# Kernel optimization log

Measured on AMD Instinct MI355X. Metric: run time of the kernel, lower is better.

## Reference

```python
import jax, jax.numpy as jnp
import numpy as np

N_NODES = 50000
N_EDGES = 800000
IN_F, OUT_F, N_HEADS = 128, 64, 4
NEG_SLOPE = 0.2
EPS = 1e-12


def setup_inputs() -> dict:
    key = jax.random.key(0)
    ks = jax.random.split(key, 6)
    x = jax.random.normal(ks[0], (N_NODES, IN_F), dtype=jnp.float32)
    edge_index = jax.random.randint(ks[1], (2, N_EDGES), 0, N_NODES, dtype=jnp.int32)
    # xavier-uniform-like scaled params
    W = jax.random.normal(ks[2], (IN_F, OUT_F), dtype=jnp.float32) * (2.0 / (IN_F + OUT_F)) ** 0.5
    a_l = jax.random.normal(ks[3], (OUT_F, N_HEADS), dtype=jnp.float32) * (2.0 / (OUT_F + N_HEADS)) ** 0.5
    a_r = jax.random.normal(ks[4], (OUT_F, N_HEADS), dtype=jnp.float32) * (2.0 / (OUT_F + N_HEADS)) ** 0.5
    b = jnp.zeros((OUT_F,), dtype=jnp.float32)
    return {"x": x, "edge_index": edge_index, "W": W, "a_l": a_l, "a_r": a_r, "b": b}


def reference(x, edge_index, W, a_l, a_r, b):
    # GATConv forward (eval mode: attn dropout is identity).
    # Dense NxNxH scatter + L1 normalize in the original == per-row edge softmax
    # over exp(leaky_relu(el[row]+er[col])); honor edge sparsity directly.
    n = x.shape[0]
    h = x @ W                      # [N, D] node representations
    el = h @ a_l                   # [N, H] left (dst/row) scores
    er = h @ a_r                   # [N, H] right (src/col) scores
    row, col = edge_index[0], edge_index[1]
    e = el[row] + er[col]          # [E, H]
    e = jnp.where(e > 0, e, NEG_SLOPE * e)   # leaky_relu(0.2)
    e = jnp.exp(e)
    denom = jax.ops.segment_sum(e, row, num_segments=n)        # [N, H]
    attn = e / jnp.maximum(denom[row], EPS)                    # [E, H] L1-normalized per row
    msg = attn[:, :, None] * h[col][:, None, :]                # [E, H, D]
    out = jax.ops.segment_sum(msg, row, num_segments=n)        # [N, H, D]
    out = out + b                                              # bias broadcast over heads
    return out.reshape(n, -1)                                  # [N, H*D]
```

## Files before the change

### kernel.cpp

```cpp
#include <hip/hip_runtime.h>

#define N_NODES 50000
#define N_EDGES 800000
#define IN_F    128
#define OUT_F   64
#define N_HEADS 4
#define NEG_SLOPE 0.2f
#define EPS 1e-12f

#define NODE_BLOCKS 782
#define NB   196
#define NCH  784
#define S2N  (NB * NCH)
#define S2B  151

typedef __attribute__((ext_vector_type(8))) short bf16x8;
typedef __attribute__((ext_vector_type(4))) float f32x4;

__device__ __forceinline__ unsigned short f2bf(float f) {
    unsigned int u = __float_as_uint(f);
    u += 0x7FFFu + ((u >> 16) & 1u);
    return (unsigned short)(u >> 16);
}

__global__ __launch_bounds__(256) void k_init(
    const float* __restrict__ W, unsigned short* __restrict__ Wt,
    const int* __restrict__ row, int* __restrict__ histG)
{
    __shared__ int hist[NB];
    const int bb = blockIdx.x;
    const int t = threadIdx.x;
    if (bb < 4) {
        int i = bb * 256 + t;
        for (; i < OUT_F * IN_F; i += 4 * 256) {
            int c = i >> 7, k = i & 127;
            Wt[i] = f2bf(W[k * OUT_F + c]);
        }
        return;
    }
    const int ch = bb - 4;
    if (t < NB) hist[t] = 0;
    __syncthreads();
    const int e0 = ch * 1024 + t * 4;
    if (e0 + 3 < N_EDGES) {
        int4 r4 = *(const int4*)(row + e0);
        atomicAdd(&hist[r4.x >> 8], 1);
        atomicAdd(&hist[r4.y >> 8], 1);
        atomicAdd(&hist[r4.z >> 8], 1);
        atomicAdd(&hist[r4.w >> 8], 1);
    } else {
        #pragma unroll
        for (int j = 0; j < 4; ++j)
            if (e0 + j < N_EDGES) atomicAdd(&hist[row[e0 + j] >> 8], 1);
    }
    __syncthreads();
    if (t < NB) histG[t * NCH + ch] = hist[t];
}

__global__ __launch_bounds__(256) void k_h_el_er(
    const float* __restrict__ x, const unsigned short* __restrict__ Wt,
    const float* __restrict__ a_l, const float* __restrict__ a_r,
    unsigned short* __restrict__ h_bf,
    float* __restrict__ el, float* __restrict__ er)
{
    __shared__ unsigned short xs[64 * 128];
    __shared__ unsigned short wsh[64 * 128];
    const int tid = threadIdx.x;
    const int node0 = blockIdx.x * 64;

    {
        const uint4* src = (const uint4*)Wt;
        #pragma unroll
        for (int j = 0; j < 4; ++j) {
            int idx = tid + 256 * j;
            int r = idx >> 4;
            int cb = (idx & 15) << 4;
            uint4 v = src[idx];
            *(uint4*)((char*)wsh + r * 256 + (cb ^ ((r & 7) << 4))) = v;
        }
    }
    {
        const int r = tid >> 2;
        const int c0 = (tid & 3) * 32;
        const int node = node0 + r;
        unsigned int pk[16];
        if (node < N_NODES) {
            const float* src = x + (size_t)node * IN_F + c0;
            #pragma unroll
            for (int i = 0; i < 8; ++i) {
                float4 v = *(const float4*)(src + 4 * i);
                pk[2 * i + 0] = (unsigned)f2bf(v.x) | ((unsigned)f2bf(v.y) << 16);
                pk[2 * i + 1] = (unsigned)f2bf(v.z) | ((unsigned)f2bf(v.w) << 16);
            }
        } else {
            #pragma unroll
            for (int i = 0; i < 16; ++i) pk[i] = 0;
        }
        #pragma unroll
        for (int q = 0; q < 4; ++q) {
            int cb = c0 * 2 + q * 16;
            *(uint4*)((char*)xs + r * 256 + (cb ^ ((r & 7) << 4))) =
                make_uint4(pk[4 * q], pk[4 * q + 1], pk[4 * q + 2], pk[4 * q + 3]);
        }
    }
    __syncthreads();

    const int w  = tid >> 6, l = tid & 63;
    const int lr = l & 15, lg = l >> 4;
    const int arow = w * 16 + lr;

    bf16x8 afr[4];
    #pragma unroll
    for (int t = 0; t < 4; ++t) {
        int cb = t * 64 + lg * 16;
        afr[t] = *(const bf16x8*)((char*)xs + arow * 256 + (cb ^ ((arow & 7) << 4)));
    }

    const f32x4 zero = {0.f, 0.f, 0.f, 0.f};
    f32x4 acc[4] = {zero, zero, zero, zero};
    #pragma unroll
    for (int nt = 0; nt < 4; ++nt) {
        const int brow = nt * 16 + lr;
        #pragma unroll
        for (int t = 0; t < 4; ++t) {
            int cb = t * 64 + lg * 16;
            bf16x8 bfr = *(const bf16x8*)((char*)wsh + brow * 256 + (cb ^ ((brow & 7) << 4)));
            acc[nt] = __builtin_amdgcn_mfma_f32_16x16x32_bf16(afr[t], bfr, acc[nt], 0, 0, 0);
        }
    }

    #pragma unroll
    for (int r = 0; r < 4; ++r) {
        const int node = node0 + w * 16 + lg * 4 + r;
        if (node < N_NODES) {
            #pragma unroll
            for (int nt = 0; nt < 4; ++nt)
                h_bf[(size_t)node * OUT_F + nt * 16 + lr] = f2bf(acc[nt][r]);
        }
    }

    float4 al4[4], ar4[4];
    #pragma unroll
    for (int nt = 0; nt < 4; ++nt) {
        al4[nt] = *(const float4*)(a_l + (size_t)(nt * 16 + lr) * N_HEADS);
        ar4[nt] = *(const float4*)(a_r + (size_t)(nt * 16 + lr) * N_HEADS);
    }
    #pragma unroll
    for (int r = 0; r < 4; ++r) {
        float4 pl = make_float4(0.f, 0.f, 0.f, 0.f);
        float4 pr = make_float4(0.f, 0.f, 0.f, 0.f);
        #pragma unroll
        for (int nt = 0; nt < 4; ++nt) {
            const float v = acc[nt][r];
            pl.x += v * al4[nt].x; pl.y += v * al4[nt].y;
            pl.z += v * al4[nt].z; pl.w += v * al4[nt].w;
            pr.x += v * ar4[nt].x; pr.y += v * ar4[nt].y;
            pr.z += v * ar4[nt].z; pr.w += v * ar4[nt].w;
        }
        #pragma unroll
        for (int off = 1; off < 16; off <<= 1) {
            pl.x += __shfl_xor(pl.x, off); pl.y += __shfl_xor(pl.y, off);
            pl.z += __shfl_xor(pl.z, off); pl.w += __shfl_xor(pl.w, off);
            pr.x += __shfl_xor(pr.x, off); pr.y += __shfl_xor(pr.y, off);
            pr.z += __shfl_xor(pr.z, off); pr.w += __shfl_xor(pr.w, off);
        }
        const int node = node0 + w * 16 + lg * 4 + r;
        if (lr == 0 && node < N_NODES) {
            *(float4*)(el + (size_t)node * N_HEADS) = pl;
            *(float4*)(er + (size_t)node * N_HEADS) = pr;
        }
    }
}

__global__ __launch_bounds__(256) void k_scan2_local(
    const int* __restrict__ histG, int* __restrict__ scanHist,
    int* __restrict__ blocksum)
{
    __shared__ int wsum[4];
    const int t = threadIdx.x;
    const int base = blockIdx.x * 1024 + t * 4;

    int4 d = make_int4(0, 0, 0, 0);
    if (base + 3 < S2N) d = *(const int4*)(histG + base);
    else {
        if (base + 0 < S2N) d.x = histG[base + 0];
        if (base + 1 < S2N) d.y = histG[base + 1];
        if (base + 2 < S2N) d.z = histG[base + 2];
        if (base + 3 < S2N) d.w = histG[base + 3];
    }
    const int tsum = d.x + d.y + d.z + d.w;

    const int lane = t & 63, wave = t >> 6;
    int inc = tsum;
    #pragma unroll
    for (int off = 1; off < 64; off <<= 1) {
        int v = __shfl_up(inc, off);
        if (lane >= off) inc += v;
    }
    if (lane == 63) wsum[wave] = inc;
    __syncthreads();

    int woff = 0;
    #pragma unroll
    for (int w = 0; w < 4; ++w) woff += (w < wave) ? wsum[w] : 0;

    const int ex = woff + inc - tsum;
    int4 o;
    o.x = ex; o.y = ex + d.x; o.z = o.y + d.y; o.w = o.z + d.z;
    if (base + 3 < S2N) *(int4*)(scanHist + base) = o;
    else {
        if (base + 0 < S2N) scanHist[base + 0] = o.x;
        if (base + 1 < S2N) scanHist[base + 1] = o.y;
        if (base + 2 < S2N) scanHist[base + 2] = o.z;
        if (base + 3 < S2N) scanHist[base + 3] = o.w;
    }
    if (t == 0) blocksum[blockIdx.x] = wsum[0] + wsum[1] + wsum[2] + wsum[3];
}

__global__ __launch_bounds__(256) void k_scan2_add(
    const int* __restrict__ blocksum, int* __restrict__ scanHist)
{
    const int bb = blockIdx.x;
    int off = 0;
    for (int i = 0; i < bb; ++i) off += blocksum[i];
    if (off == 0) return;

    const int t = threadIdx.x;
    const int base = bb * 1024 + t * 4;
    if (base + 3 < S2N) {
        int4 v = *(int4*)(scanHist + base);
        v.x += off; v.y += off; v.z += off; v.w += off;
        *(int4*)(scanHist + base) = v;
    } else {
        if (base + 0 < S2N) scanHist[base + 0] += off;
        if (base + 1 < S2N) scanHist[base + 1] += off;
        if (base + 2 < S2N) scanHist[base + 2] += off;
        if (base + 3 < S2N) scanHist[base + 3] += off;
    }
}

__global__ __launch_bounds__(256) void k_scatter(
    const int* __restrict__ row, const int* __restrict__ col,
    const int* __restrict__ scanHist, unsigned* __restrict__ ebuf)
{
    __shared__ int off[NB];
    const int ch = blockIdx.x;
    const int t = threadIdx.x;
    if (t < NB) off[t] = scanHist[t * NCH + ch];
    __syncthreads();
    const int e0 = ch * 1024;
    #pragma unroll
    for (int k = 0; k < 4; ++k) {
        const int e = e0 + t + k * 256;
        if (e < N_EDGES) {
            const int r = row[e], c = col[e];
            const int pos = atomicAdd(&off[r >> 8], 1);
            ebuf[pos] = ((unsigned)(r & 255) << 17) | (unsigned)c;
        }
    }
}

__global__ __launch_bounds__(256) void k_bucket(
    const unsigned* __restrict__ ebuf, const int* __restrict__ scanHist,
    int* __restrict__ rowptr, int* __restrict__ csr_col)
{
    __shared__ int cnt[256];
    __shared__ int wsum[4];
    const int b = blockIdx.x;
    const int t = threadIdx.x;
    const int base = scanHist[b * NCH];
    const int end  = (b < NB - 1) ? scanHist[(b + 1) * NCH] : N_EDGES;

    cnt[t] = 0;
    __syncthreads();
    for (int i = base + t; i < end; i += 256)
        atomicAdd(&cnt[ebuf[i] >> 17], 1);
    __syncthreads();

    const int val = cnt[t];
    const int lane = t & 63, wave = t >> 6;
    int inc = val;
    #pragma unroll
    for (int off = 1; off < 64; off <<= 1) {
        int v = __shfl_up(inc, off);
        if (lane >= off) inc += v;
    }
    if (lane == 63) wsum[wave] = inc;
    __syncthreads();
    int woff = 0;
    #pragma unroll
    for (int w = 0; w < 4; ++w) woff += (w < wave) ? wsum[w] : 0;
    const int excl = base + woff + inc - val;

    const int node = (b << 8) + t;
    if (node < N_NODES) rowptr[node] = excl;
    if (b == NB - 1 && t == 0) rowptr[N_NODES] = N_EDGES;
    __syncthreads();
    cnt[t] = excl;
    __syncthreads();

    for (int i = base + t; i < end; i += 256) {
        const unsigned p = ebuf[i];
        const int pos = atomicAdd(&cnt[p >> 17], 1);
        csr_col[pos] = (int)(p & 0x1FFFFu);
    }
}

__global__ __launch_bounds__(256) void k_gather(
    const int* __restrict__ rowptr, const int* __restrict__ csr_col,
    const float* __restrict__ el, const float* __restrict__ er,
    const unsigned short* __restrict__ h_bf, const float* __restrict__ b,
    float* __restrict__ out)
{
    int n = blockIdx.x * 4 + (threadIdx.x >> 6);
    if (n >= N_NODES) return;
    const int lane = threadIdx.x & 63;
    const int g    = lane >> 4;
    const int fq   = lane & 15;

    const int s0 = rowptr[n], s1 = rowptr[n + 1];
    const int deg = s1 - s0;
    const int nit = (deg + 3) >> 2;

    float acc[4][4];
    #pragma unroll
    for (int hd = 0; hd < 4; ++hd)
        #pragma unroll
        for (int f = 0; f < 4; ++f) acc[hd][f] = 0.f;
    float den[4] = {0.f, 0.f, 0.f, 0.f};

    const float4 elv = *reinterpret_cast<const float4*>(el + ((unsigned)n << 2));

    bool v_cur = false;
    float4 erv_cur = make_float4(0.f, 0.f, 0.f, 0.f);
    uint2  h_cur = make_uint2(0, 0);
    if (nit > 0) {
        const int j = s0 + g;
        v_cur = j < s1;
        const int jc = v_cur ? j : (s1 - 1);
        const int c = csr_col[jc];
        erv_cur = *reinterpret_cast<const float4*>(er + ((unsigned)c << 2));
        h_cur   = *reinterpret_cast<const uint2*>(h_bf + (((unsigned)c << 6) + (fq << 2)));
    }

    for (int it = 0; it < nit; ++it) {
        bool v_nx = false;
        float4 erv_nx = make_float4(0.f, 0.f, 0.f, 0.f);
        uint2  h_nx = make_uint2(0, 0);
        if (it + 1 < nit) {
            const int j = s0 + (it + 1) * 4 + g;
            v_nx = j < s1;
            const int jc = v_nx ? j : (s1 - 1);
            const int c = csr_col[jc];
            erv_nx = *reinterpret_cast<const float4*>(er + ((unsigned)c << 2));
            h_nx   = *reinterpret_cast<const uint2*>(h_bf + (((unsigned)c << 6) + (fq << 2)));
        }

        float t0 = elv.x + erv_cur.x, t1 = elv.y + erv_cur.y;
        float t2 = elv.z + erv_cur.z, t3 = elv.w + erv_cur.w;
        t0 = t0 > 0.f ? t0 : NEG_SLOPE * t0;
        t1 = t1 > 0.f ? t1 : NEG_SLOPE * t1;
        t2 = t2 > 0.f ? t2 : NEG_SLOPE * t2;
        t3 = t3 > 0.f ? t3 : NEG_SLOPE * t3;
        float4 w = make_float4(__expf(t0), __expf(t1), __expf(t2), __expf(t3));
        if (!v_cur) w = make_float4(0.f, 0.f, 0.f, 0.f);

        const float h0 = __uint_as_float(h_cur.x << 16);
        const float h1 = __uint_as_float(h_cur.x & 0xFFFF0000u);
        const float h2 = __uint_as_float(h_cur.y << 16);
        const float h3 = __uint_as_float(h_cur.y & 0xFFFF0000u);

        den[0] += w.x; den[1] += w.y; den[2] += w.z; den[3] += w.w;
        acc[0][0] += w.x * h0; acc[0][1] += w.x * h1; acc[0][2] += w.x * h2; acc[0][3] += w.x * h3;
        acc[1][0] += w.y * h0; acc[1][1] += w.y * h1; acc[1][2] += w.y * h2; acc[1][3] += w.y * h3;
        acc[2][0] += w.z * h0; acc[2][1] += w.z * h1; acc[2][2] += w.z * h2; acc[2][3] += w.z * h3;
        acc[3][0] += w.w * h0; acc[3][1] += w.w * h1; acc[3][2] += w.w * h2; acc[3][3] += w.w * h3;

        v_cur = v_nx; erv_cur = erv_nx; h_cur = h_nx;
    }

    #pragma unroll
    for (int hd = 0; hd < 4; ++hd) {
        float v = den[hd];
        v += __shfl_xor(v, 16); v += __shfl_xor(v, 32);
        den[hd] = v;
        #pragma unroll
        for (int f = 0; f < 4; ++f) {
            float u = acc[hd][f];
            u += __shfl_xor(u, 16); u += __shfl_xor(u, 32);
            acc[hd][f] = u;
        }
    }

    const float dg = g == 0 ? den[0] : g == 1 ? den[1] : g == 2 ? den[2] : den[3];
    const float inv = 1.f / fmaxf(dg, EPS);
    float4 o;
    o.x = (g == 0 ? acc[0][0] : g == 1 ? acc[1][0] : g == 2 ? acc[2][0] : acc[3][0]);
    o.y = (g == 0 ? acc[0][1] : g == 1 ? acc[1][1] : g == 2 ? acc[2][1] : acc[3][1]);
    o.z = (g == 0 ? acc[0][2] : g == 1 ? acc[1][2] : g == 2 ? acc[2][2] : acc[3][2]);
    o.w = (g == 0 ? acc[0][3] : g == 1 ? acc[1][3] : g == 2 ? acc[2][3] : acc[3][3]);

    const float4 bias = *(const float4*)(b + fq * 4);
    o.x = o.x * inv + bias.x;
    o.y = o.y * inv + bias.y;
    o.z = o.z * inv + bias.z;
    o.w = o.w * inv + bias.w;
    *(float4*)(out + (size_t)n * (N_HEADS * OUT_F) + g * 64 + fq * 4) = o;
}

extern "C" void kernel_launch(void* const* d_in, const int* in_sizes, int n_in,
                              void* d_out, int out_size, void* d_ws, size_t ws_size,
                              hipStream_t stream)
{
    const float* x   = (const float*)d_in[0];
    const int*   ei  = (const int*)d_in[1];
    const float* W   = (const float*)d_in[2];
    const float* a_l = (const float*)d_in[3];
    const float* a_r = (const float*)d_in[4];
    const float* b   = (const float*)d_in[5];
    float* out = (float*)d_out;

    char* ws = (char*)d_ws;
    unsigned short* h_bf = (unsigned short*)(ws);
    float*    el       = (float*)   (ws +  6400000);
    float*    er       = (float*)   (ws +  7200000);
    unsigned short* Wt = (unsigned short*)(ws + 8000000);
    int*      histG    = (int*)     (ws +  8016384);
    int*      scanHist = (int*)     (ws +  8631040);
    int*      blocksum = (int*)     (ws +  9245696);
    unsigned* ebuf     = (unsigned*)(ws +  9246720);
    int*      csr_col  = (int*)     (ws + 12446720);
    int*      rowptr   = (int*)     (ws + 15646720);

    const int* row = ei;
    const int* col = ei + N_EDGES;

    k_init      <<<4 + NCH, 256, 0, stream>>>(W, Wt, row, histG);
    k_h_el_er   <<<NODE_BLOCKS, 256, 0, stream>>>(x, Wt, a_l, a_r, h_bf, el, er);
    k_scan2_local<<<S2B, 256, 0, stream>>>(histG, scanHist, blocksum);
    k_scan2_add <<<S2B, 256, 0, stream>>>(blocksum, scanHist);
    k_scatter   <<<NCH, 256, 0, stream>>>(row, col, scanHist, ebuf);
    k_bucket    <<<NB, 256, 0, stream>>>(ebuf, scanHist, rowptr, csr_col);
    k_gather    <<<N_NODES / 4, 256, 0, stream>>>(rowptr, csr_col, el, er, h_bf, b, out);
}
```

Measured before the change: 93.54 us.

## Precompute edge attention weights in bucket pass and deepen gather prefetch

```diff
diff --git a/kernel.cpp b/kernel.cpp
--- a/kernel.cpp
+++ b/kernel.cpp
@@ -9,10 +9,11 @@
 #define EPS 1e-12f
 
 #define NODE_BLOCKS 782
-#define NB   196
-#define NCH  784
-#define S2N  (NB * NCH)
-#define S2B  151
+#define NB    391
+#define CHUNK 2048
+#define NCH   391
+#define S2N   (NB * NCH)
+#define S2B   150
 
 typedef __attribute__((ext_vector_type(8))) short bf16x8;
 typedef __attribute__((ext_vector_type(4))) float f32x4;
@@ -39,22 +40,23 @@
         return;
     }
     const int ch = bb - 4;
-    if (t < NB) hist[t] = 0;
-    __syncthreads();
-    const int e0 = ch * 1024 + t * 4;
-    if (e0 + 3 < N_EDGES) {
-        int4 r4 = *(const int4*)(row + e0);
-        atomicAdd(&hist[r4.x >> 8], 1);
-        atomicAdd(&hist[r4.y >> 8], 1);
-        atomicAdd(&hist[r4.z >> 8], 1);
-        atomicAdd(&hist[r4.w >> 8], 1);
+    for (int i = t; i < NB; i += 256) hist[i] = 0;
+    __syncthreads();
+    const int e0 = ch * CHUNK + t * 8;
+    if (e0 + 7 < N_EDGES) {
+        int4 a = *(const int4*)(row + e0);
+        int4 c = *(const int4*)(row + e0 + 4);
+        atomicAdd(&hist[a.x >> 7], 1); atomicAdd(&hist[a.y >> 7], 1);
+        atomicAdd(&hist[a.z >> 7], 1); atomicAdd(&hist[a.w >> 7], 1);
+        atomicAdd(&hist[c.x >> 7], 1); atomicAdd(&hist[c.y >> 7], 1);
+        atomicAdd(&hist[c.z >> 7], 1); atomicAdd(&hist[c.w >> 7], 1);
     } else {
         #pragma unroll
-        for (int j = 0; j < 4; ++j)
-            if (e0 + j < N_EDGES) atomicAdd(&hist[row[e0 + j] >> 8], 1);
-    }
-    __syncthreads();
-    if (t < NB) histG[t * NCH + ch] = hist[t];
+        for (int j = 0; j < 8; ++j)
+            if (e0 + j < N_EDGES) atomicAdd(&hist[row[e0 + j] >> 7], 1);
+    }
+    __syncthreads();
+    for (int i = t; i < NB; i += 256) histG[i * NCH + ch] = hist[i];
 }
 
 __global__ __launch_bounds__(256) void k_h_el_er(
@@ -246,69 +248,92 @@
     __shared__ int off[NB];
     const int ch = blockIdx.x;
     const int t = threadIdx.x;
-    if (t < NB) off[t] = scanHist[t * NCH + ch];
-    __syncthreads();
-    const int e0 = ch * 1024;
-    #pragma unroll
-    for (int k = 0; k < 4; ++k) {
+    for (int i = t; i < NB; i += 256) off[i] = scanHist[i * NCH + ch];
+    __syncthreads();
+    const int e0 = ch * CHUNK;
+    #pragma unroll
+    for (int k = 0; k < 8; ++k) {
         const int e = e0 + t + k * 256;
         if (e < N_EDGES) {
             const int r = row[e], c = col[e];
-            const int pos = atomicAdd(&off[r >> 8], 1);
-            ebuf[pos] = ((unsigned)(r & 255) << 17) | (unsigned)c;
+            const int pos = atomicAdd(&off[r >> 7], 1);
+            ebuf[pos] = ((unsigned)(r & 127) << 17) | (unsigned)c;
         }
     }
 }
 
 __global__ __launch_bounds__(256) void k_bucket(
     const unsigned* __restrict__ ebuf, const int* __restrict__ scanHist,
-    int* __restrict__ rowptr, int* __restrict__ csr_col)
-{
-    __shared__ int cnt[256];
-    __shared__ int wsum[4];
+    const float* __restrict__ el, const float* __restrict__ er,
+    int* __restrict__ rowptr, int* __restrict__ csr_col,
+    float4* __restrict__ csr_w)
+{
+    __shared__ float4 elv[128];
+    __shared__ int cnt[128];
+    __shared__ int wsum2[2];
     const int b = blockIdx.x;
     const int t = threadIdx.x;
+    const int node0 = b << 7;
     const int base = scanHist[b * NCH];
     const int end  = (b < NB - 1) ? scanHist[(b + 1) * NCH] : N_EDGES;
 
-    cnt[t] = 0;
+    if (t < 128) {
+        const int node = node0 + t;
+        elv[t] = (node < N_NODES) ? *(const float4*)(el + node * 4)
+                                  : make_float4(0.f, 0.f, 0.f, 0.f);
+        cnt[t] = 0;
+    }
     __syncthreads();
     for (int i = base + t; i < end; i += 256)
         atomicAdd(&cnt[ebuf[i] >> 17], 1);
     __syncthreads();
 
-    const int val = cnt[t];
+    int inc = 0, val = 0;
     const int lane = t & 63, wave = t >> 6;
-    int inc = val;
-    #pragma unroll
-    for (int off = 1; off < 64; off <<= 1) {
-        int v = __shfl_up(inc, off);
-        if (lane >= off) inc += v;
-    }
-    if (lane == 63) wsum[wave] = inc;
-    __syncthreads();
-    int woff = 0;
-    #pragma unroll
-    for (int w = 0; w < 4; ++w) woff += (w < wave) ? wsum[w] : 0;
-    const int excl = base + woff + inc - val;
-
-    const int node = (b << 8) + t;
-    if (node < N_NODES) rowptr[node] = excl;
+    if (t < 128) {
+        val = cnt[t];
+        inc = val;
+        #pragma unroll
+        for (int off = 1; off < 64; off <<= 1) {
+            int v = __shfl_up(inc, off);
+            if (lane >= off) inc += v;
+        }
+        if (lane == 63) wsum2[wave] = inc;
+    }
+    __syncthreads();
+    int excl = 0;
+    if (t < 128) {
+        const int woff = (wave == 1) ? wsum2[0] : 0;
+        excl = base + woff + inc - val;
+        const int node = node0 + t;
+        if (node < N_NODES) rowptr[node] = excl;
+    }
     if (b == NB - 1 && t == 0) rowptr[N_NODES] = N_EDGES;
     __syncthreads();
-    cnt[t] = excl;
+    if (t < 128) cnt[t] = excl;
     __syncthreads();
 
     for (int i = base + t; i < end; i += 256) {
         const unsigned p = ebuf[i];
-        const int pos = atomicAdd(&cnt[p >> 17], 1);
-        csr_col[pos] = (int)(p & 0x1FFFFu);
+        const int r = p >> 17;
+        const int c = (int)(p & 0x1FFFFu);
+        const int pos = atomicAdd(&cnt[r], 1);
+        const float4 e4 = elv[r];
+        const float4 r4 = *(const float4*)(er + ((unsigned)c << 2));
+        float s0 = e4.x + r4.x, s1 = e4.y + r4.y;
+        float s2 = e4.z + r4.z, s3 = e4.w + r4.w;
+        s0 = s0 > 0.f ? s0 : NEG_SLOPE * s0;
+        s1 = s1 > 0.f ? s1 : NEG_SLOPE * s1;
+        s2 = s2 > 0.f ? s2 : NEG_SLOPE * s2;
+        s3 = s3 > 0.f ? s3 : NEG_SLOPE * s3;
+        csr_col[pos] = c;
+        csr_w[pos] = make_float4(__expf(s0), __expf(s1), __expf(s2), __expf(s3));
     }
 }
 
 __global__ __launch_bounds__(256) void k_gather(
     const int* __restrict__ rowptr, const int* __restrict__ csr_col,
-    const float* __restrict__ el, const float* __restrict__ er,
+    const float4* __restrict__ csr_w,
     const unsigned short* __restrict__ h_bf, const float* __restrict__ b,
     float* __restrict__ out)
 {
@@ -319,8 +344,7 @@
     const int fq   = lane & 15;
 
     const int s0 = rowptr[n], s1 = rowptr[n + 1];
-    const int deg = s1 - s0;
-    const int nit = (deg + 3) >> 2;
+    const int nit = (s1 - s0 + 3) >> 2;
 
     float acc[4][4];
     #pragma unroll
@@ -329,55 +353,41 @@
         for (int f = 0; f < 4; ++f) acc[hd][f] = 0.f;
     float den[4] = {0.f, 0.f, 0.f, 0.f};
 
-    const float4 elv = *reinterpret_cast<const float4*>(el + ((unsigned)n << 2));
-
-    bool v_cur = false;
-    float4 erv_cur = make_float4(0.f, 0.f, 0.f, 0.f);
-    uint2  h_cur = make_uint2(0, 0);
-    if (nit > 0) {
-        const int j = s0 + g;
-        v_cur = j < s1;
-        const int jc = v_cur ? j : (s1 - 1);
-        const int c = csr_col[jc];
-        erv_cur = *reinterpret_cast<const float4*>(er + ((unsigned)c << 2));
-        h_cur   = *reinterpret_cast<const uint2*>(h_bf + (((unsigned)c << 6) + (fq << 2)));
-    }
+#define GLOAD(ii, WV, HV)                                                  \
+    {                                                                      \
+        WV = make_float4(0.f, 0.f, 0.f, 0.f);                              \
+        HV = make_uint2(0u, 0u);                                           \
+        const int j = s0 + (ii) * 4 + g;                                   \
+        if ((ii) < nit && j < s1) {                                        \
+            const int c = csr_col[j];                                      \
+            WV = csr_w[j];                                                 \
+            HV = *(const uint2*)(h_bf + (((unsigned)c << 6) + (fq << 2))); \
+        }                                                                  \
+    }
+
+    float4 w0, w1; uint2 h0, h1;
+    GLOAD(0, w0, h0);
+    GLOAD(1, w1, h1);
 
     for (int it = 0; it < nit; ++it) {
-        bool v_nx = false;
-        float4 erv_nx = make_float4(0.f, 0.f, 0.f, 0.f);
-        uint2  h_nx = make_uint2(0, 0);
-        if (it + 1 < nit) {
-            const int j = s0 + (it + 1) * 4 + g;
-            v_nx = j < s1;
-            const int jc = v_nx ? j : (s1 - 1);
-            const int c = csr_col[jc];
-            erv_nx = *reinterpret_cast<const float4*>(er + ((unsigned)c << 2));
-            h_nx   = *reinterpret_cast<const uint2*>(h_bf + (((unsigned)c << 6) + (fq << 2)));
-        }
-
-        float t0 = elv.x + erv_cur.x, t1 = elv.y + erv_cur.y;
-        float t2 = elv.z + erv_cur.z, t3 = elv.w + erv_cur.w;
-        t0 = t0 > 0.f ? t0 : NEG_SLOPE * t0;
-        t1 = t1 > 0.f ? t1 : NEG_SLOPE * t1;
-        t2 = t2 > 0.f ? t2 : NEG_SLOPE * t2;
-        t3 = t3 > 0.f ? t3 : NEG_SLOPE * t3;
-        float4 w = make_float4(__expf(t0), __expf(t1), __expf(t2), __expf(t3));
-        if (!v_cur) w = make_float4(0.f, 0.f, 0.f, 0.f);
-
-        const float h0 = __uint_as_float(h_cur.x << 16);
-        const float h1 = __uint_as_float(h_cur.x & 0xFFFF0000u);
-        const float h2 = __uint_as_float(h_cur.y << 16);
-        const float h3 = __uint_as_float(h_cur.y & 0xFFFF0000u);
-
-        den[0] += w.x; den[1] += w.y; den[2] += w.z; den[3] += w.w;
-        acc[0][0] += w.x * h0; acc[0][1] += w.x * h1; acc[0][2] += w.x * h2; acc[0][3] += w.x * h3;
-        acc[1][0] += w.y * h0; acc[1][1] += w.y * h1; acc[1][2] += w.y * h2; acc[1][3] += w.y * h3;
-        acc[2][0] += w.z * h0; acc[2][1] += w.z * h1; acc[2][2] += w.z * h2; acc[2][3] += w.z * h3;
-        acc[3][0] += w.w * h0; acc[3][1] += w.w * h1; acc[3][2] += w.w * h2; acc[3][3] += w.w * h3;
-
-        v_cur = v_nx; erv_cur = erv_nx; h_cur = h_nx;
-    }
+        float4 w2; uint2 h2;
+        GLOAD(it + 2, w2, h2);
+
+        const float f0 = __uint_as_float(h0.x << 16);
+        const float f1 = __uint_as_float(h0.x & 0xFFFF0000u);
+        const float f2 = __uint_as_float(h0.y << 16);
+        const float f3 = __uint_as_float(h0.y & 0xFFFF0000u);
+
+        den[0] += w0.x; den[1] += w0.y; den[2] += w0.z; den[3] += w0.w;
+        acc[0][0] += w0.x * f0; acc[0][1] += w0.x * f1; acc[0][2] += w0.x * f2; acc[0][3] += w0.x * f3;
+        acc[1][0] += w0.y * f0; acc[1][1] += w0.y * f1; acc[1][2] += w0.y * f2; acc[1][3] += w0.y * f3;
+        acc[2][0] += w0.z * f0; acc[2][1] += w0.z * f1; acc[2][2] += w0.z * f2; acc[2][3] += w0.z * f3;
+        acc[3][0] += w0.w * f0; acc[3][1] += w0.w * f1; acc[3][2] += w0.w * f2; acc[3][3] += w0.w * f3;
+
+        w0 = w1; h0 = h1;
+        w1 = w2; h1 = h2;
+    }
+#undef GLOAD
 
     #pragma unroll
     for (int hd = 0; hd < 4; ++hd) {
@@ -426,20 +436,21 @@
     float*    er       = (float*)   (ws +  7200000);
     unsigned short* Wt = (unsigned short*)(ws + 8000000);
     int*      histG    = (int*)     (ws +  8016384);
-    int*      scanHist = (int*)     (ws +  8631040);
-    int*      blocksum = (int*)     (ws +  9245696);
-    unsigned* ebuf     = (unsigned*)(ws +  9246720);
-    int*      csr_col  = (int*)     (ws + 12446720);
-    int*      rowptr   = (int*)     (ws + 15646720);
+    int*      scanHist = (int*)     (ws +  8627920);
+    int*      blocksum = (int*)     (ws +  9239456);
+    unsigned* ebuf     = (unsigned*)(ws +  9240480);
+    int*      csr_col  = (int*)     (ws + 12440480);
+    float4*   csr_w    = (float4*)  (ws + 15640496);
+    int*      rowptr   = (int*)     (ws + 28440496);
 
     const int* row = ei;
     const int* col = ei + N_EDGES;
 
-    k_init      <<<4 + NCH, 256, 0, stream>>>(W, Wt, row, histG);
-    k_h_el_er   <<<NODE_BLOCKS, 256, 0, stream>>>(x, Wt, a_l, a_r, h_bf, el, er);
+    k_init       <<<4 + NCH, 256, 0, stream>>>(W, Wt, row, histG);
+    k_h_el_er    <<<NODE_BLOCKS, 256, 0, stream>>>(x, Wt, a_l, a_r, h_bf, el, er);
     k_scan2_local<<<S2B, 256, 0, stream>>>(histG, scanHist, blocksum);
-    k_scan2_add <<<S2B, 256, 0, stream>>>(blocksum, scanHist);
-    k_scatter   <<<NCH, 256, 0, stream>>>(row, col, scanHist, ebuf);
-    k_bucket    <<<NB, 256, 0, stream>>>(ebuf, scanHist, rowptr, csr_col);
-    k_gather    <<<N_NODES / 4, 256, 0, stream>>>(rowptr, csr_col, el, er, h_bf, b, out);
-}
+    k_scan2_add  <<<S2B, 256, 0, stream>>>(blocksum, scanHist);
+    k_scatter    <<<NCH, 256, 0, stream>>>(row, col, scanHist, ebuf);
+    k_bucket     <<<NB, 256, 0, stream>>>(ebuf, scanHist, el, er, rowptr, csr_col, csr_w);
+    k_gather     <<<N_NODES / 4, 256, 0, stream>>>(rowptr, csr_col, csr_w, h_bf, b, out);
+}
```

After: 92.81 us. Within noise of the previous version (-0.8%).
